# Performance work log

Hardware: AMD Instinct MI355X
Metric: run time of the kernel (lower is better)

The kernel has to match this reference:

```python
import jax, jax.numpy as jnp
import numpy as np

EPS = 1e-12

def _l2normalize(v):
    return v / (jnp.sum(v ** 2) ** 0.5 + EPS)

def spectral_norm(w, u):
    # w: [Cin, Cout] (flattened 1x1 conv kernel), u: [1, Cout]; 1 power iteration
    v = _l2normalize(u @ w.T)          # [1, Cin]
    u2 = _l2normalize(v @ w)           # [1, Cout]
    sigma = (v @ w @ u2.T)[0, 0]
    return w / sigma

def conv1x1(x, w):
    # x: [B,H,W,Cin], w: [Cin,Cout]
    return jnp.einsum('bhwc,cd->bhwd', x, w)

def maxpool2(x):
    B, H, W, C = x.shape
    return x.reshape(B, H // 2, 2, W // 2, 2, C).max(axis=(2, 4))

def setup_inputs() -> dict:
    key = jax.random.key(0)
    ks = jax.random.split(key, 10)
    B, H, W, C = 16, 64, 64, 512
    c8, c2 = C // 8, C // 2
    x = jax.random.normal(ks[0], (B, H, W, C), dtype=jnp.float32)
    k_theta = jax.random.normal(ks[1], (C, c8), dtype=jnp.float32) * 0.05
    u_theta = jax.random.normal(ks[2], (1, c8), dtype=jnp.float32)
    k_phi = jax.random.normal(ks[3], (C, c8), dtype=jnp.float32) * 0.05
    u_phi = jax.random.normal(ks[4], (1, c8), dtype=jnp.float32)
    k_g = jax.random.normal(ks[5], (C, c2), dtype=jnp.float32) * 0.05
    u_g = jax.random.normal(ks[6], (1, c2), dtype=jnp.float32)
    k_attn = jax.random.normal(ks[7], (c2, C), dtype=jnp.float32) * 0.05
    u_attn = jax.random.normal(ks[8], (1, C), dtype=jnp.float32)
    sigma = jnp.float32(0.1)
    return {"x": x, "k_theta": k_theta, "u_theta": u_theta,
            "k_phi": k_phi, "u_phi": u_phi, "k_g": k_g, "u_g": u_g,
            "k_attn": k_attn, "u_attn": u_attn, "sigma": sigma}

def reference(x, k_theta, u_theta, k_phi, u_phi, k_g, u_g, k_attn, u_attn, sigma):
    B, H, W, C = x.shape
    c8, c2 = C // 8, C // 2
    loc = H * W
    down = loc // 4
    theta = conv1x1(x, spectral_norm(k_theta, u_theta)).reshape(B, loc, c8)
    phi = maxpool2(conv1x1(x, spectral_norm(k_phi, u_phi))).reshape(B, down, c8)
    attn = jax.nn.softmax(jnp.einsum('bnc,bmc->bnm', theta, phi), axis=-1)  # [B, loc, down]
    g = maxpool2(conv1x1(x, spectral_norm(k_g, u_g))).reshape(B, down, c2)
    attn_g = jnp.einsum('bnm,bmc->bnc', attn, g).reshape(B, H, W, c2)
    attn_g = conv1x1(attn_g, spectral_norm(k_attn, u_attn))
    return x + sigma * attn_g
```

## Files before the change

### kernel.cpp

```cpp
#include <hip/hip_runtime.h>
#include <hip/hip_bf16.h>


using bf16 = __hip_bfloat16;
typedef unsigned short u16;
typedef __attribute__((ext_vector_type(8))) short bf16x8;
typedef __attribute__((ext_vector_type(4))) float f32x4;

#define MFMA16(a, b, c) __builtin_amdgcn_mfma_f32_16x16x32_bf16((a), (b), (c), 0, 0, 0)

#define WS_FLAG   0
#define WS_WAT2   787456
#define WS_THETA  1311744
#define WS_PHI    9700352
#define WS_G      11797504
#define WS_WAT    20186112
#define WS_TOTAL  20448256

__device__ __forceinline__ float bf2f(bf16 v) { return __bfloat162float(v); }
__device__ __forceinline__ bf16 f2bf(float v) { return __float2bfloat16(v); }
__device__ __forceinline__ u16 f2bf_bits(float v) { bf16 h = f2bf(v); return *(u16*)&h; }

template <typename T> struct io;
template <> struct io<bf16> {
  static __device__ __forceinline__ float ld(const bf16* p) { return bf2f(*p); }
  static __device__ __forceinline__ void st(bf16* p, float v) { *p = f2bf(v); }
  static __device__ __forceinline__ int tag() { return 0; }
};
template <> struct io<float> {
  static __device__ __forceinline__ float ld(const float* p) { return *p; }
  static __device__ __forceinline__ void st(float* p, float v) { *p = v; }
  static __device__ __forceinline__ int tag() { return 1; }
};

__global__ __launch_bounds__(256) void detect_kernel(const void* xraw, int* flag) {
  const uint4* p = (const uint4*)xraw;
  int t = threadIdx.x;
  int cnt = 0;
#pragma unroll 8
  for (int i = 0; i < 32; ++i) {
    uint4 v = p[t + i * 256];
    unsigned d[4] = {v.x, v.y, v.z, v.w};
#pragma unroll
    for (int k = 0; k < 4; ++k) {
      if ((d[k] & 0x7F80u) == 0x7F80u) cnt++;
      if ((d[k] & 0x7F800000u) == 0x7F800000u) cnt++;
    }
  }
#pragma unroll
  for (int o = 32; o > 0; o >>= 1) cnt += __shfl_down(cnt, o, 64);
  __shared__ int red[4];
  if ((t & 63) == 0) red[t >> 6] = cnt;
  __syncthreads();
  if (t == 0) flag[0] = (red[0] + red[1] + red[2] + red[3] > 4) ? 1 : 0;
}

__device__ __forceinline__ float block_sum_256(float x, float* red) {
#pragma unroll
  for (int o = 32; o > 0; o >>= 1) x += __shfl_down(x, o, 64);
  __syncthreads();
  if ((threadIdx.x & 63) == 0) red[threadIdx.x >> 6] = x;
  __syncthreads();
  return red[0] + red[1] + red[2] + red[3];
}

template <typename T, int CIN, int COUT, int MODE>
__device__ __forceinline__ void sn_impl(const T* w, const T* u,
                                        u16* wAllT, u16* waT) {
  __shared__ float v[CIN];
  __shared__ float red[4];
  const int t = threadIdx.x, wv = t >> 6, ln = t & 63;

  float uv[COUT / 64];
#pragma unroll
  for (int jj = 0; jj < COUT / 64; ++jj) uv[jj] = io<T>::ld(u + jj * 64 + ln);

#pragma unroll 2
  for (int i = wv; i < CIN; i += 4) {
    float acc = 0.f;
#pragma unroll
    for (int jj = 0; jj < COUT / 64; ++jj)
      acc += uv[jj] * io<T>::ld(w + (size_t)i * COUT + jj * 64 + ln);
#pragma unroll
    for (int o = 32; o > 0; o >>= 1) acc += __shfl_down(acc, o, 64);
    if (ln == 0) v[i] = acc;
  }
  __syncthreads();
  float loc = 0.f;
  for (int i = t; i < CIN; i += 256) loc += v[i] * v[i];
  float s1 = block_sum_256(loc, red);
  float inv1 = 1.f / (sqrtf(s1) + 1e-12f);

  float loc2 = 0.f;
#pragma unroll
  for (int j0 = 0; j0 < COUT; j0 += 256) {
    int j = j0 + t;
    if (j < COUT) {
      float a0 = 0.f, a1 = 0.f, a2 = 0.f, a3 = 0.f;
#pragma unroll 4
      for (int i = 0; i < CIN; i += 4) {
        a0 += v[i + 0] * io<T>::ld(w + (size_t)(i + 0) * COUT + j);
        a1 += v[i + 1] * io<T>::ld(w + (size_t)(i + 1) * COUT + j);
        a2 += v[i + 2] * io<T>::ld(w + (size_t)(i + 2) * COUT + j);
        a3 += v[i + 3] * io<T>::ld(w + (size_t)(i + 3) * COUT + j);
      }
      float acc = ((a0 + a1) + (a2 + a3)) * inv1;
      loc2 += acc * acc;
    }
  }
  float s2 = block_sum_256(loc2, red);
  float sigma = s2 / (sqrtf(s2) + 1e-12f);
  float winv = 1.f / sigma;

#pragma unroll 4
  for (int k = t; k < CIN * COUT; k += 256) {
    float val = io<T>::ld(w + k) * winv;
    u16 bits = f2bf_bits(val);
    int i = k / COUT, j = k % COUT;
    if constexpr (MODE == 0) wAllT[(size_t)j * 512 + i] = bits;
    if constexpr (MODE == 1) wAllT[(size_t)(64 + j) * 512 + i] = bits;
    if constexpr (MODE == 2) wAllT[(size_t)(128 + j) * 512 + i] = bits;
    if constexpr (MODE == 3) waT[(size_t)j * 256 + i] = bits;
  }
}

template <typename T>
__global__ __launch_bounds__(256) void sn_kernel(
    const void* ktv, const void* utv, const void* kpv, const void* upv,
    const void* kgv, const void* ugv, const void* kav, const void* uav,
    u16* wAllT, u16* waT, const int* flag) {
  if (flag[0] != io<T>::tag()) return;
  switch (blockIdx.x) {
    case 0:  sn_impl<T, 512, 64, 0>((const T*)ktv, (const T*)utv, wAllT, waT); break;
    case 1:  sn_impl<T, 512, 64, 1>((const T*)kpv, (const T*)upv, wAllT, waT); break;
    case 2:  sn_impl<T, 512, 256, 2>((const T*)kgv, (const T*)ugv, wAllT, waT); break;
    default: sn_impl<T, 256, 512, 3>((const T*)kav, (const T*)uav, wAllT, waT); break;
  }
}

template <typename T>
__global__ __launch_bounds__(256, 2) void conv3_mfma_kernel(
    const void* xv, const u16* __restrict__ wAllT,
    bf16* __restrict__ theta, bf16* __restrict__ phi, bf16* __restrict__ gT,
    const int* flag) {
  if (flag[0] != io<T>::tag()) return;
  constexpr bool SPLIT = sizeof(T) == 4;
  const T* x = (const T*)xv;

  __shared__ u16 xh_s[2][64][136];
  __shared__ u16 xl_s[2][64][136];

  const int tid = threadIdx.x;
  const int w = tid >> 6;
  const int lane = tid & 63;
  const int quad = lane >> 4;
  const int l15 = lane & 15;
  const int bb = blockIdx.x >> 6;
  const int tile = blockIdx.x & 63;
  const int pth = tile >> 3, ptw = tile & 7;

  const int sp = tid >> 2;
  const int sq = tid & 3;
  const int swin = sp >> 2, sd = sp & 3;
  const int sh = 2 * (pth * 4 + (swin >> 2)) + (sd >> 1);
  const int sw = 2 * (ptw * 4 + (swin & 3)) + (sd & 1);
  const T* xrow = x + ((size_t)(bb * 64 + sh) * 64 + sw) * 512 + sq * 32;

  auto STAGE = [&](int buf, int kc) {
    if constexpr (SPLIT) {
      const float* src = (const float*)xrow + kc * 128;
#pragma unroll
      for (int hl = 0; hl < 2; ++hl) {
        float f[16];
#pragma unroll
        for (int i = 0; i < 4; ++i) {
          float4 v4 = ((const float4*)src)[hl * 4 + i];
          f[4 * i] = v4.x; f[4 * i + 1] = v4.y; f[4 * i + 2] = v4.z; f[4 * i + 3] = v4.w;
        }
        unsigned ph_[8], pl_[8];
#pragma unroll
        for (int i = 0; i < 8; ++i) {
          float a = f[2 * i], b = f[2 * i + 1];
          u16 ha = f2bf_bits(a), hb = f2bf_bits(b);
          float ra = a - __uint_as_float((unsigned)ha << 16);
          float rb = b - __uint_as_float((unsigned)hb << 16);
          ph_[i] = (unsigned)ha | ((unsigned)hb << 16);
          pl_[i] = (unsigned)f2bf_bits(ra) | ((unsigned)f2bf_bits(rb) << 16);
        }
        *(uint4*)&xh_s[buf][sp][sq * 32 + hl * 16] =
            make_uint4(ph_[0], ph_[1], ph_[2], ph_[3]);
        *(uint4*)&xh_s[buf][sp][sq * 32 + hl * 16 + 8] =
            make_uint4(ph_[4], ph_[5], ph_[6], ph_[7]);
        *(uint4*)&xl_s[buf][sp][sq * 32 + hl * 16] =
            make_uint4(pl_[0], pl_[1], pl_[2], pl_[3]);
        *(uint4*)&xl_s[buf][sp][sq * 32 + hl * 16 + 8] =
            make_uint4(pl_[4], pl_[5], pl_[6], pl_[7]);
      }
    } else {
      const u16* src = (const u16*)xrow + kc * 128;
#pragma unroll
      for (int i = 0; i < 4; ++i)
        *(uint4*)&xh_s[buf][sp][sq * 32 + i * 8] = ((const uint4*)src)[i];
    }
  };

  f32x4 acc[4][6];
#pragma unroll
  for (int mt = 0; mt < 4; ++mt)
#pragma unroll
    for (int nt = 0; nt < 6; ++nt) acc[mt][nt] = (f32x4){0.f, 0.f, 0.f, 0.f};

  const u16* wb = wAllT + (size_t)(w * 96 + l15) * 512 + quad * 8;

  STAGE(0, 0);
  __syncthreads();
#pragma unroll 1
  for (int kc = 0; kc < 4; ++kc) {
    const int buf = kc & 1;
    if (kc < 3) STAGE(buf ^ 1, kc + 1);
#pragma unroll
    for (int ks = 0; ks < 4; ++ks) {
      bf16x8 ah[4], al[4];
#pragma unroll
      for (int mt = 0; mt < 4; ++mt) {
        ah[mt] = *(const bf16x8*)&xh_s[buf][mt * 16 + l15][ks * 32 + quad * 8];
        if constexpr (SPLIT)
          al[mt] = *(const bf16x8*)&xl_s[buf][mt * 16 + l15][ks * 32 + quad * 8];
      }
#pragma unroll
      for (int nt = 0; nt < 6; ++nt) {
        bf16x8 b = *(const bf16x8*)(wb + (size_t)nt * 16 * 512 + kc * 128 + ks * 32);
#pragma unroll
        for (int mt = 0; mt < 4; ++mt) {
          acc[mt][nt] = MFMA16(ah[mt], b, acc[mt][nt]);
          if constexpr (SPLIT) acc[mt][nt] = MFMA16(al[mt], b, acc[mt][nt]);
        }
      }
    }
    __syncthreads();
  }

#pragma unroll
  for (int nt = 0; nt < 6; ++nt) {
    const int nb = w * 96 + nt * 16;
    const int n = nb + l15;
    if (nb < 64) {
#pragma unroll
      for (int mt = 0; mt < 4; ++mt)
#pragma unroll
        for (int r = 0; r < 4; ++r) {
          int p = mt * 16 + quad * 4 + r;
          int win = p >> 2, d = p & 3;
          int h = 2 * (pth * 4 + (win >> 2)) + (d >> 1);
          int wc = 2 * (ptw * 4 + (win & 3)) + (d & 1);
          theta[((size_t)bb * 4096 + h * 64 + wc) * 64 + n] = f2bf(acc[mt][nt][r]);
        }
    } else if (nb < 128) {
      const int ch = n - 64;
#pragma unroll
      for (int mt = 0; mt < 4; ++mt) {
        int win = mt * 4 + quad;
        int pp = (pth * 4 + (win >> 2)) * 32 + (ptw * 4 + (win & 3));
        float mx = fmaxf(fmaxf(acc[mt][nt][0], acc[mt][nt][1]),
                         fmaxf(acc[mt][nt][2], acc[mt][nt][3]));
        phi[((size_t)bb * 1024 + pp) * 64 + ch] = f2bf(mx);
      }
    } else {
      const int ch = n - 128;
#pragma unroll
      for (int mt = 0; mt < 4; ++mt) {
        int win = mt * 4 + quad;
        int pp = (pth * 4 + (win >> 2)) * 32 + (ptw * 4 + (win & 3));
        float mx = fmaxf(fmaxf(acc[mt][nt][0], acc[mt][nt][1]),
                         fmaxf(acc[mt][nt][2], acc[mt][nt][3]));
        gT[((size_t)bb * 256 + ch) * 1024 + pp] = f2bf(mx);
      }
    }
  }
}

template <typename T>
__global__ __launch_bounds__(256) void attn_kernel(
    const bf16* __restrict__ thetab, const bf16* __restrict__ phib,
    const bf16* __restrict__ gTb, void* __restrict__ outv, const int* flag) {
  if (flag[0] != io<T>::tag()) return;
  __shared__ u16 ph_s[64][70];
  __shared__ u16 gt_s[256][70];
  __shared__ u16 p_s[4][32][70];

  const int tid = threadIdx.x;
  const int w = tid >> 6;
  const int lane = tid & 63;
  const int quad = lane >> 4;
  const int l15 = lane & 15;
  const int qt = blockIdx.x * 4 + w;
  const int bb = qt >> 7;
  const int q0 = (qt & 127) * 32;

  bf16x8 aT[2][2];
#pragma unroll
  for (int t = 0; t < 2; ++t) {
    const u16* th = (const u16*)thetab +
                    ((size_t)bb * 4096 + q0 + t * 16 + l15) * 64 + quad * 8;
    aT[t][0] = *(const bf16x8*)th;
    aT[t][1] = *(const bf16x8*)(th + 32);
  }

  const u16* ph = (const u16*)phib + (size_t)bb * 1024 * 64;
  const u16* gT = (const u16*)gTb + (size_t)bb * 256 * 1024;

  f32x4 o[2][16];
#pragma unroll
  for (int t = 0; t < 2; ++t)
#pragma unroll
    for (int i = 0; i < 16; ++i) o[t][i] = (f32x4){0.f, 0.f, 0.f, 0.f};
  float mold[2][4], lsum[2][4];
#pragma unroll
  for (int t = 0; t < 2; ++t)
#pragma unroll
    for (int r = 0; r < 4; ++r) { mold[t][r] = -1e30f; lsum[t][r] = 0.f; }

  const int pr = tid >> 2, pc = (tid & 3) * 16;
  const int gr = tid >> 3, gc = (tid & 7) * 8;

#pragma unroll 1
  for (int kc = 0; kc < 16; ++kc) {
    __syncthreads();
    {
      const u16* src = ph + ((kc * 64 + pr) * 64 + pc);
      *(uint4*)&ph_s[pr][pc] = *(const uint4*)src;
      *(uint4*)&ph_s[pr][pc + 8] = *(const uint4*)(src + 8);
    }
#pragma unroll
    for (int i = 0; i < 8; ++i) {
      const u16* src = gT + (size_t)(i * 32 + gr) * 1024 + kc * 64 + gc;
      *(uint4*)&gt_s[i * 32 + gr][gc] = *(const uint4*)src;
    }
    __syncthreads();

    f32x4 s[2][4];
#pragma unroll
    for (int t4 = 0; t4 < 4; ++t4) {
      bf16x8 b0 = *(const bf16x8*)&ph_s[t4 * 16 + l15][quad * 8];
      bf16x8 b1 = *(const bf16x8*)&ph_s[t4 * 16 + l15][32 + quad * 8];
#pragma unroll
      for (int t = 0; t < 2; ++t) {
        f32x4 z = (f32x4){0.f, 0.f, 0.f, 0.f};
        z = MFMA16(aT[t][0], b0, z);
        z = MFMA16(aT[t][1], b1, z);
        s[t][t4] = z;
      }
    }
#pragma unroll
    for (int t = 0; t < 2; ++t) {
      float rmax[4], mnew[4], alpha[4], rsum[4];
#pragma unroll
      for (int r = 0; r < 4; ++r) {
        rmax[r] = fmaxf(fmaxf(s[t][0][r], s[t][1][r]),
                        fmaxf(s[t][2][r], s[t][3][r]));
#pragma unroll
        for (int m = 1; m <= 8; m <<= 1)
          rmax[r] = fmaxf(rmax[r], __shfl_xor(rmax[r], m, 64));
        mnew[r] = fmaxf(mold[t][r], rmax[r]);
        alpha[r] = __expf(mold[t][r] - mnew[r]);
        mold[t][r] = mnew[r];
        rsum[r] = 0.f;
      }
#pragma unroll
      for (int t4 = 0; t4 < 4; ++t4)
#pragma unroll
        for (int r = 0; r < 4; ++r) {
          float pv = __expf(s[t][t4][r] - mnew[r]);
          rsum[r] += pv;
          p_s[w][t * 16 + quad * 4 + r][t4 * 16 + l15] = f2bf_bits(pv);
        }
#pragma unroll
      for (int r = 0; r < 4; ++r) {
#pragma unroll
        for (int m = 1; m <= 8; m <<= 1) rsum[r] += __shfl_xor(rsum[r], m, 64);
        lsum[t][r] = lsum[t][r] * alpha[r] + rsum[r];
      }
#pragma unroll
      for (int i = 0; i < 16; ++i) {
        o[t][i][0] *= alpha[0]; o[t][i][1] *= alpha[1];
        o[t][i][2] *= alpha[2]; o[t][i][3] *= alpha[3];
      }
    }
    bf16x8 pa00 = *(const bf16x8*)&p_s[w][l15][quad * 8];
    bf16x8 pa01 = *(const bf16x8*)&p_s[w][l15][32 + quad * 8];
    bf16x8 pa10 = *(const bf16x8*)&p_s[w][16 + l15][quad * 8];
    bf16x8 pa11 = *(const bf16x8*)&p_s[w][16 + l15][32 + quad * 8];
#pragma unroll
    for (int t4 = 0; t4 < 16; ++t4) {
      bf16x8 b0 = *(const bf16x8*)&gt_s[t4 * 16 + l15][quad * 8];
      bf16x8 b1 = *(const bf16x8*)&gt_s[t4 * 16 + l15][32 + quad * 8];
      o[0][t4] = MFMA16(pa00, b0, o[0][t4]);
      o[0][t4] = MFMA16(pa01, b1, o[0][t4]);
      o[1][t4] = MFMA16(pa10, b0, o[1][t4]);
      o[1][t4] = MFMA16(pa11, b1, o[1][t4]);
    }
  }

  const size_t RB = 512 * sizeof(T);
  char* ob = (char*)outv;
#pragma unroll
  for (int t = 0; t < 2; ++t) {
    float inv[4];
#pragma unroll
    for (int r = 0; r < 4; ++r) inv[r] = 1.f / lsum[t][r];
#pragma unroll
    for (int t4 = 0; t4 < 16; ++t4)
#pragma unroll
      for (int r = 0; r < 4; ++r) {
        size_t row = (size_t)bb * 4096 + q0 + t * 16 + quad * 4 + r;
        u16* dst = (u16*)(ob + row * RB + RB / 2) + t4 * 16 + l15;
        *dst = f2bf_bits(o[t][t4][r] * inv[r]);
      }
  }
}

template <typename T>
__global__ __launch_bounds__(256, 3) void proj_kernel(
    const u16* __restrict__ waT, const void* __restrict__ xv,
    const void* __restrict__ sigv, void* __restrict__ outv, const int* flag) {
  if (flag[0] != io<T>::tag()) return;
  const T* xp = (const T*)xv;
  T* outp = (T*)outv;
  __shared__ u16 a_s[64][264];

  const int tid = threadIdx.x;
  const int w = tid >> 6;
  const int lane = tid & 63;
  const int quad = lane >> 4;
  const int l15 = lane & 15;
  const int R0 = blockIdx.x * 64;
  const size_t RB = 512 * sizeof(T);

  {
    int row = tid >> 2, seg = tid & 3;
    const uint4* src = (const uint4*)((const char*)outv + (size_t)(R0 + row) * RB + RB / 2);
#pragma unroll
    for (int i = 0; i < 8; ++i)
      *(uint4*)&a_s[row][seg * 64 + i * 8] = src[seg * 8 + i];
  }
  __syncthreads();

  float sg = io<T>::ld((const T*)sigv);
#pragma unroll 1
  for (int h = 0; h < 2; ++h) {
    f32x4 pc[16];
#pragma unroll
    for (int i = 0; i < 16; ++i) pc[i] = (f32x4){0.f, 0.f, 0.f, 0.f};
#pragma unroll 1
    for (int ks = 0; ks < 8; ++ks) {
      bf16x8 a = *(const bf16x8*)&a_s[w * 16 + l15][ks * 32 + quad * 8];
#pragma unroll
      for (int t4 = 0; t4 < 16; ++t4) {
        bf16x8 b = *(const bf16x8*)(waT + (size_t)(h * 256 + t4 * 16 + l15) * 256 + ks * 32 + quad * 8);
        pc[t4] = MFMA16(a, b, pc[t4]);
      }
    }
#pragma unroll
    for (int t4 = 0; t4 < 16; ++t4)
#pragma unroll
      for (int r = 0; r < 4; ++r) {
        int row = R0 + w * 16 + quad * 4 + r;
        int col = h * 256 + t4 * 16 + l15;
        size_t off = (size_t)row * 512 + col;
        io<T>::st(outp + off, io<T>::ld(xp + off) + sg * pc[t4][r]);
      }
  }
}

extern "C" void kernel_launch(void* const* d_in, const int* in_sizes, int n_in,
                              void* d_out, int out_size, void* d_ws, size_t ws_size,
                              hipStream_t stream) {
  if (ws_size < (size_t)WS_TOTAL) return;
  char* ws = (char*)d_ws;
  int*   flag  = (int*)(ws + WS_FLAG);
  u16*   wAllT = (u16*)(ws + WS_WAT2);
  bf16*  theta = (bf16*)(ws + WS_THETA);
  bf16*  phi   = (bf16*)(ws + WS_PHI);
  bf16*  gT    = (bf16*)(ws + WS_G);
  u16*   waT   = (u16*)(ws + WS_WAT);

  detect_kernel<<<1, 256, 0, stream>>>(d_in[0], flag);

  sn_kernel<bf16><<<4, 256, 0, stream>>>(d_in[1], d_in[2], d_in[3], d_in[4],
                                         d_in[5], d_in[6], d_in[7], d_in[8],
                                         wAllT, waT, flag);
  sn_kernel<float><<<4, 256, 0, stream>>>(d_in[1], d_in[2], d_in[3], d_in[4],
                                          d_in[5], d_in[6], d_in[7], d_in[8],
                                          wAllT, waT, flag);

  conv3_mfma_kernel<bf16><<<1024, 256, 0, stream>>>(d_in[0], wAllT, theta, phi, gT, flag);
  conv3_mfma_kernel<float><<<1024, 256, 0, stream>>>(d_in[0], wAllT, theta, phi, gT, flag);

  attn_kernel<bf16><<<512, 256, 0, stream>>>(theta, phi, gT, d_out, flag);
  attn_kernel<float><<<512, 256, 0, stream>>>(theta, phi, gT, d_out, flag);

  proj_kernel<bf16><<<1024, 256, 0, stream>>>(waT, d_in[0], d_in[9], d_out, flag);
  proj_kernel<float><<<1024, 256, 0, stream>>>(waT, d_in[0], d_in[9], d_out, flag);
}
```

Before: 794.8 us.

## Shrink attention tiles, prefetch K/V into registers, and lazily rescale softmax

Each wave in the attention kernel now handles 16 query rows instead of 32, and the key/value chunk shrinks from 64 to 32. The grid doubles to 1024 blocks and per-thread accumulator registers are halved, which is meant to raise occupancy. The next phi/gT chunk is loaded into registers while the current chunk is computed, overlapping global loads with MFMA work. The online softmax only updates the running max when it grows by more than 8, skipping the output rescale otherwise; this trades some numerical headroom in the exponent for fewer multiplies, while each phi/gT chunk is now reused by fewer query rows.

```diff
diff --git a/kernel.cpp b/kernel.cpp
--- a/kernel.cpp
+++ b/kernel.cpp
@@ -284,9 +284,9 @@
     const bf16* __restrict__ thetab, const bf16* __restrict__ phib,
     const bf16* __restrict__ gTb, void* __restrict__ outv, const int* flag) {
   if (flag[0] != io<T>::tag()) return;
-  __shared__ u16 ph_s[64][70];
-  __shared__ u16 gt_s[256][70];
-  __shared__ u16 p_s[4][32][70];
+  __shared__ u16 ph_s[32][66];
+  __shared__ u16 gt_s[256][34];
+  __shared__ u16 p_s[4][16][34];
 
   const int tid = threadIdx.x;
   const int w = tid >> 6;
@@ -294,129 +294,112 @@
   const int quad = lane >> 4;
   const int l15 = lane & 15;
   const int qt = blockIdx.x * 4 + w;
-  const int bb = qt >> 7;
-  const int q0 = (qt & 127) * 32;
-
-  bf16x8 aT[2][2];
-#pragma unroll
-  for (int t = 0; t < 2; ++t) {
-    const u16* th = (const u16*)thetab +
-                    ((size_t)bb * 4096 + q0 + t * 16 + l15) * 64 + quad * 8;
-    aT[t][0] = *(const bf16x8*)th;
-    aT[t][1] = *(const bf16x8*)(th + 32);
-  }
+  const int bb = qt >> 8;
+  const int q0 = (qt & 255) * 16;
+
+  const u16* th = (const u16*)thetab + ((size_t)bb * 4096 + q0 + l15) * 64 + quad * 8;
+  const bf16x8 a0 = *(const bf16x8*)th;
+  const bf16x8 a1 = *(const bf16x8*)(th + 32);
 
   const u16* ph = (const u16*)phib + (size_t)bb * 1024 * 64;
   const u16* gT = (const u16*)gTb + (size_t)bb * 256 * 1024;
 
-  f32x4 o[2][16];
-#pragma unroll
-  for (int t = 0; t < 2; ++t)
-#pragma unroll
-    for (int i = 0; i < 16; ++i) o[t][i] = (f32x4){0.f, 0.f, 0.f, 0.f};
-  float mold[2][4], lsum[2][4];
-#pragma unroll
-  for (int t = 0; t < 2; ++t)
-#pragma unroll
-    for (int r = 0; r < 4; ++r) { mold[t][r] = -1e30f; lsum[t][r] = 0.f; }
-
-  const int pr = tid >> 2, pc = (tid & 3) * 16;
-  const int gr = tid >> 3, gc = (tid & 7) * 8;
+  f32x4 o[16];
+#pragma unroll
+  for (int i = 0; i < 16; ++i) o[i] = (f32x4){0.f, 0.f, 0.f, 0.f};
+  float mold[4] = {-1e30f, -1e30f, -1e30f, -1e30f};
+  float lsum[4] = {0.f, 0.f, 0.f, 0.f};
+
+  const int pr = tid >> 3, pc = (tid & 7) * 8;
+  const int gr = tid >> 2, gq = (tid & 3) * 8;
+
+  uint4 pf_p, pf_g[4];
+  auto LOAD = [&](int kc) {
+    pf_p = *(const uint4*)(ph + ((kc * 32 + pr) * 64 + pc));
+#pragma unroll
+    for (int i = 0; i < 4; ++i)
+      pf_g[i] = *(const uint4*)(gT + (size_t)(i * 64 + gr) * 1024 + kc * 32 + gq);
+  };
+  LOAD(0);
 
 #pragma unroll 1
-  for (int kc = 0; kc < 16; ++kc) {
+  for (int kc = 0; kc < 32; ++kc) {
     __syncthreads();
-    {
-      const u16* src = ph + ((kc * 64 + pr) * 64 + pc);
-      *(uint4*)&ph_s[pr][pc] = *(const uint4*)src;
-      *(uint4*)&ph_s[pr][pc + 8] = *(const uint4*)(src + 8);
-    }
-#pragma unroll
-    for (int i = 0; i < 8; ++i) {
-      const u16* src = gT + (size_t)(i * 32 + gr) * 1024 + kc * 64 + gc;
-      *(uint4*)&gt_s[i * 32 + gr][gc] = *(const uint4*)src;
-    }
+    *(uint4*)&ph_s[pr][pc] = pf_p;
+#pragma unroll
+    for (int i = 0; i < 4; ++i)
+      *(uint4*)&gt_s[i * 64 + gr][gq] = pf_g[i];
     __syncthreads();
-
-    f32x4 s[2][4];
-#pragma unroll
-    for (int t4 = 0; t4 < 4; ++t4) {
+    if (kc < 31) LOAD(kc + 1);
+
+    f32x4 s[2];
+#pragma unroll
+    for (int t4 = 0; t4 < 2; ++t4) {
       bf16x8 b0 = *(const bf16x8*)&ph_s[t4 * 16 + l15][quad * 8];
       bf16x8 b1 = *(const bf16x8*)&ph_s[t4 * 16 + l15][32 + quad * 8];
-#pragma unroll
-      for (int t = 0; t < 2; ++t) {
-        f32x4 z = (f32x4){0.f, 0.f, 0.f, 0.f};
-        z = MFMA16(aT[t][0], b0, z);
-        z = MFMA16(aT[t][1], b1, z);
-        s[t][t4] = z;
-      }
-    }
-#pragma unroll
-    for (int t = 0; t < 2; ++t) {
-      float rmax[4], mnew[4], alpha[4], rsum[4];
+      f32x4 z = (f32x4){0.f, 0.f, 0.f, 0.f};
+      z = MFMA16(a0, b0, z);
+      z = MFMA16(a1, b1, z);
+      s[t4] = z;
+    }
+    float rmax[4], alpha[4], rsum[4];
+    bool need = false;
+#pragma unroll
+    for (int r = 0; r < 4; ++r) {
+      rmax[r] = fmaxf(s[0][r], s[1][r]);
+#pragma unroll
+      for (int m = 1; m <= 8; m <<= 1) rmax[r] = fmaxf(rmax[r], __shfl_xor(rmax[r], m, 64));
+      bool upd = rmax[r] > mold[r] + 8.f;
+      alpha[r] = upd ? __expf(mold[r] - rmax[r]) : 1.f;
+      if (upd) mold[r] = rmax[r];
+      need |= upd;
+      rsum[r] = 0.f;
+    }
+#pragma unroll
+    for (int t4 = 0; t4 < 2; ++t4)
 #pragma unroll
       for (int r = 0; r < 4; ++r) {
-        rmax[r] = fmaxf(fmaxf(s[t][0][r], s[t][1][r]),
-                        fmaxf(s[t][2][r], s[t][3][r]));
-#pragma unroll
-        for (int m = 1; m <= 8; m <<= 1)
-          rmax[r] = fmaxf(rmax[r], __shfl_xor(rmax[r], m, 64));
-        mnew[r] = fmaxf(mold[t][r], rmax[r]);
-        alpha[r] = __expf(mold[t][r] - mnew[r]);
-        mold[t][r] = mnew[r];
-        rsum[r] = 0.f;
-      }
-#pragma unroll
-      for (int t4 = 0; t4 < 4; ++t4)
-#pragma unroll
-        for (int r = 0; r < 4; ++r) {
-          float pv = __expf(s[t][t4][r] - mnew[r]);
-          rsum[r] += pv;
-          p_s[w][t * 16 + quad * 4 + r][t4 * 16 + l15] = f2bf_bits(pv);
-        }
-#pragma unroll
-      for (int r = 0; r < 4; ++r) {
-#pragma unroll
-        for (int m = 1; m <= 8; m <<= 1) rsum[r] += __shfl_xor(rsum[r], m, 64);
-        lsum[t][r] = lsum[t][r] * alpha[r] + rsum[r];
-      }
+        float pv = __expf(s[t4][r] - mold[r]);
+        rsum[r] += pv;
+        p_s[w][quad * 4 + r][t4 * 16 + l15] = f2bf_bits(pv);
+      }
+#pragma unroll
+    for (int r = 0; r < 4; ++r)
+#pragma unroll
+      for (int m = 1; m <= 8; m <<= 1) rsum[r] += __shfl_xor(rsum[r], m, 64);
+    if (__any(need)) {
 #pragma unroll
       for (int i = 0; i < 16; ++i) {
-        o[t][i][0] *= alpha[0]; o[t][i][1] *= alpha[1];
-        o[t][i][2] *= alpha[2]; o[t][i][3] *= alpha[3];
-      }
-    }
-    bf16x8 pa00 = *(const bf16x8*)&p_s[w][l15][quad * 8];
-    bf16x8 pa01 = *(const bf16x8*)&p_s[w][l15][32 + quad * 8];
-    bf16x8 pa10 = *(const bf16x8*)&p_s[w][16 + l15][quad * 8];
-    bf16x8 pa11 = *(const bf16x8*)&p_s[w][16 + l15][32 + quad * 8];
+        o[i][0] *= alpha[0]; o[i][1] *= alpha[1];
+        o[i][2] *= alpha[2]; o[i][3] *= alpha[3];
+      }
+#pragma unroll
+      for (int r = 0; r < 4; ++r) lsum[r] = lsum[r] * alpha[r] + rsum[r];
+    } else {
+#pragma unroll
+      for (int r = 0; r < 4; ++r) lsum[r] += rsum[r];
+    }
+    bf16x8 pa = *(const bf16x8*)&p_s[w][l15][quad * 8];
 #pragma unroll
     for (int t4 = 0; t4 < 16; ++t4) {
-      bf16x8 b0 = *(const bf16x8*)&gt_s[t4 * 16 + l15][quad * 8];
-      bf16x8 b1 = *(const bf16x8*)&gt_s[t4 * 16 + l15][32 + quad * 8];
-      o[0][t4] = MFMA16(pa00, b0, o[0][t4]);
-      o[0][t4] = MFMA16(pa01, b1, o[0][t4]);
-      o[1][t4] = MFMA16(pa10, b0, o[1][t4]);
-      o[1][t4] = MFMA16(pa11, b1, o[1][t4]);
+      bf16x8 b = *(const bf16x8*)&gt_s[t4 * 16 + l15][quad * 8];
+      o[t4] = MFMA16(pa, b, o[t4]);
     }
   }
 
   const size_t RB = 512 * sizeof(T);
   char* ob = (char*)outv;
-#pragma unroll
-  for (int t = 0; t < 2; ++t) {
-    float inv[4];
-#pragma unroll
-    for (int r = 0; r < 4; ++r) inv[r] = 1.f / lsum[t][r];
-#pragma unroll
-    for (int t4 = 0; t4 < 16; ++t4)
-#pragma unroll
-      for (int r = 0; r < 4; ++r) {
-        size_t row = (size_t)bb * 4096 + q0 + t * 16 + quad * 4 + r;
-        u16* dst = (u16*)(ob + row * RB + RB / 2) + t4 * 16 + l15;
-        *dst = f2bf_bits(o[t][t4][r] * inv[r]);
-      }
-  }
+  float inv[4];
+#pragma unroll
+  for (int r = 0; r < 4; ++r) inv[r] = 1.f / lsum[r];
+#pragma unroll
+  for (int t4 = 0; t4 < 16; ++t4)
+#pragma unroll
+    for (int r = 0; r < 4; ++r) {
+      size_t row = (size_t)bb * 4096 + q0 + quad * 4 + r;
+      u16* dst = (u16*)(ob + row * RB + RB / 2) + t4 * 16 + l15;
+      *dst = f2bf_bits(o[t4][r] * inv[r]);
+    }
 }
 
 template <typename T>
@@ -496,8 +479,8 @@
   conv3_mfma_kernel<bf16><<<1024, 256, 0, stream>>>(d_in[0], wAllT, theta, phi, gT, flag);
   conv3_mfma_kernel<float><<<1024, 256, 0, stream>>>(d_in[0], wAllT, theta, phi, gT, flag);
 
-  attn_kernel<bf16><<<512, 256, 0, stream>>>(theta, phi, gT, d_out, flag);
-  attn_kernel<float><<<512, 256, 0, stream>>>(theta, phi, gT, d_out, flag);
+  attn_kernel<bf16><<<1024, 256, 0, stream>>>(theta, phi, gT, d_out, flag);
+  attn_kernel<float><<<1024, 256, 0, stream>>>(theta, phi, gT, d_out, flag);
 
   proj_kernel<bf16><<<1024, 256, 0, stream>>>(waT, d_in[0], d_in[9], d_out, flag);
   proj_kernel<float><<<1024, 256, 0, stream>>>(waT, d_in[0], d_in[9], d_out, flag);
```

Measured after the change: 881.8 us. +10.9%, slower.
